# Optimization experiments

Measured on AMD Instinct MI355X. Metric: run time of the kernel, lower is better.

The kernel has to match this reference:

```python
import jax, jax.numpy as jnp
import numpy as np

B, T, C, H = 512, 1024, 64, 128


def setup_inputs() -> dict:
    key = jax.random.key(0)
    ks = jax.random.split(key, 7)
    s = 1.0 / np.sqrt(H)  # PyTorch LSTM/Linear default init U(-1/sqrt(H), 1/sqrt(H))
    u = lambda k, shape: jax.random.uniform(k, shape, jnp.float32, -s, s)
    return {
        "x": jax.random.normal(ks[0], (B, T, C), jnp.float32),
        # Per-channel stacked LSTM params; input_size=1 so W_ih is [C, 4H]
        "W_ih": u(ks[1], (C, 4 * H)),
        "W_hh": u(ks[2], (C, 4 * H, H)),
        "b_ih": u(ks[3], (C, 4 * H)),
        "b_hh": u(ks[4], (C, 4 * H)),
        # Per-channel final Linear(H, 1)
        "W_fc": u(ks[5], (C, H)),
        "b_fc": u(ks[6], (C,)),
    }


def reference(x, W_ih, W_hh, b_ih, b_hh, W_fc, b_fc):
    # x: [B, T, C]. All channels' LSTMs run as one fused vectorized scan.
    Bx, Tx, Cx = x.shape
    Hh = W_hh.shape[-1]
    b = b_ih + b_hh  # [C, 4H]
    xt = jnp.transpose(x, (1, 0, 2))  # [T, B, C]
    h0 = jnp.zeros((Bx, Cx, Hh), x.dtype)
    c0 = jnp.zeros((Bx, Cx, Hh), x.dtype)

    def step(carry, x_t):
        h, c = carry  # each [B, C, H]
        gates = (jnp.einsum('bc,cg->bcg', x_t, W_ih)
                 + jnp.einsum('bch,cgh->bcg', h, W_hh)
                 + b)  # [B, C, 4H]
        i, f, g, o = jnp.split(gates, 4, axis=-1)  # PyTorch gate order: i, f, g, o
        i = jax.nn.sigmoid(i)
        f = jax.nn.sigmoid(f)
        g = jnp.tanh(g)
        o = jax.nn.sigmoid(o)
        c = f * c + i * g
        h = o * jnp.tanh(c)
        return (h, c), None

    (h_last, _), _ = jax.lax.scan(step, (h0, c0), xt)
    # Per-channel Linear(H, 1) on the final hidden state, then squeeze -> [B, C]
    return jnp.einsum('bch,ch->bc', h_last, W_fc) + b_fc
```

## Files before the change

kernel.cpp:

```cpp
#include <hip/hip_runtime.h>


typedef _Float16 half8 __attribute__((ext_vector_type(8)));
typedef float floatx4 __attribute__((ext_vector_type(4)));

#define LOG2E 1.44269504088896340736f

__global__ __launch_bounds__(512, 2) void lstm_fused(
    const float* __restrict__ x,
    const float* __restrict__ Wih,
    const float* __restrict__ Whh,
    const float* __restrict__ bih,
    const float* __restrict__ bhh,
    const float* __restrict__ Wfc,
    const float* __restrict__ bfc,
    float* __restrict__ out)
{
    constexpr int T = 1024, C = 64, H = 128, G = 512;
    constexpr int TC = T * C;

    __shared__ _Float16 hbuf[2][8192];

    const int bid = blockIdx.x;
    const int ch  = bid & 63;
    const int b0  = (bid >> 6) << 6;

    const int tid = threadIdx.x;
    const int w   = tid >> 6;
    const int l   = tid & 63;
    const int q   = l >> 4;
    const int li  = l & 15;

    float wihr[4], bias[4];
    half8 Wf[4][4];
#pragma unroll
    for (int ct = 0; ct < 4; ++ct) {
        const float sc = (ct == 2) ? 2.0f * LOG2E : LOG2E;
        const int col = ct * H + w * 16 + li;
        wihr[ct] = Wih[ch * G + col] * sc;
        bias[ct] = (bih[ch * G + col] + bhh[ch * G + col]) * sc;
#pragma unroll
        for (int ks = 0; ks < 4; ++ks) {
            const float* wp = &Whh[((size_t)(ch * G + col)) * H + ks * 32 + q * 8];
            half8 hv;
#pragma unroll
            for (int j = 0; j < 8; ++j) hv[j] = (_Float16)(wp[j] * sc);
            Wf[ct][ks] = hv;
        }
    }

    for (int i = tid; i < 8192; i += 512) hbuf[0][i] = (_Float16)0.0f;

    float cst[4][4];
#pragma unroll
    for (int rt = 0; rt < 4; ++rt)
#pragma unroll
        for (int r = 0; r < 4; ++r) cst[rt][r] = 0.0f;

    const int ks_w = w >> 1;
    const int qq_w = ((w & 1) << 1) + (li >> 3);
    const int j_w  = li & 7;
    const int rxor = qq_w & 3;
    int wel[4];
#pragma unroll
    for (int r = 0; r < 4; ++r)
        wel[r] = ks_w * 512 + (qq_w * 16 + q * 4 + (r ^ rxor)) * 8 + j_w;
    const int rdoff = (q * 16 + (li ^ (q & 3))) * 8;

    const float* xb = x + ch;
    const int rb0 = (b0 + q * 4) * TC;

    float xv[4][4];
#pragma unroll
    for (int rt = 0; rt < 4; ++rt)
#pragma unroll
        for (int r = 0; r < 4; ++r)
            xv[rt][r] = xb[rb0 + (rt * 16 + r) * TC];

    const float* xnp   = xb + C;
    const float* xlast = xb + (T - 1) * C;

    __syncthreads();

    auto step = [&](const _Float16* __restrict__ rb, _Float16* __restrict__ wb) {
#pragma unroll
        for (int rt = 0; rt < 4; ++rt) {
            floatx4 acc[4];
#pragma unroll
            for (int ct = 0; ct < 4; ++ct)
#pragma unroll
                for (int r = 0; r < 4; ++r)
                    acc[ct][r] = fmaf(xv[rt][r], wihr[ct], bias[ct]);

#pragma unroll
            for (int ks = 0; ks < 4; ++ks) {
                const half8 a = *(const half8*)&rb[(rt * 4 + ks) * 512 + rdoff];
#pragma unroll
                for (int ct = 0; ct < 4; ++ct)
                    acc[ct] = __builtin_amdgcn_mfma_f32_16x16x32_f16(a, Wf[ct][ks], acc[ct], 0, 0, 0);
            }

#pragma unroll
            for (int r = 0; r < 4; ++r) {
                const float ig = __builtin_amdgcn_rcpf(1.0f + __builtin_amdgcn_exp2f(-acc[0][r]));
                const float fg = __builtin_amdgcn_rcpf(1.0f + __builtin_amdgcn_exp2f(-acc[1][r]));
                const float gg = 1.0f - 2.0f * __builtin_amdgcn_rcpf(1.0f + __builtin_amdgcn_exp2f(acc[2][r]));
                const float og = __builtin_amdgcn_rcpf(1.0f + __builtin_amdgcn_exp2f(-acc[3][r]));
                const float cn = fg * cst[rt][r] + ig * gg;
                cst[rt][r] = cn;
                const float tc = 1.0f - 2.0f * __builtin_amdgcn_rcpf(
                                     1.0f + __builtin_amdgcn_exp2f(cn * (2.0f * LOG2E)));
                wb[rt * 2048 + wel[r]] = (_Float16)(og * tc);
            }
        }

#pragma unroll
        for (int rt = 0; rt < 4; ++rt)
#pragma unroll
            for (int r = 0; r < 4; ++r)
                xv[rt][r] = xnp[rb0 + (rt * 16 + r) * TC];

        __syncthreads();
    };

    for (int t = 0; t < T; t += 2) {
        step(hbuf[0], hbuf[1]);
        xnp = (xnp == xlast) ? xnp : xnp + C;
        step(hbuf[1], hbuf[0]);
        xnp = (xnp == xlast) ? xnp : xnp + C;
    }

    if (tid < 64) {
        const int row = tid;
        const int rt = row >> 4, m = row & 15;
        float s = bfc[ch];
#pragma unroll
        for (int hh = 0; hh < H; ++hh) {
            const int ks = hh >> 5, qq = (hh & 31) >> 3, j = hh & 7;
            const int c = qq * 16 + (m ^ (qq & 3));
            s += (float)hbuf[0][(rt * 4 + ks) * 512 + c * 8 + j] * Wfc[ch * H + hh];
        }
        out[(size_t)(b0 + row) * C + ch] = s;
    }
}

extern "C" void kernel_launch(void* const* d_in, const int* in_sizes, int n_in,
                              void* d_out, int out_size, void* d_ws, size_t ws_size,
                              hipStream_t stream) {
    const float* x   = (const float*)d_in[0];
    const float* Wih = (const float*)d_in[1];
    const float* Whh = (const float*)d_in[2];
    const float* bih = (const float*)d_in[3];
    const float* bhh = (const float*)d_in[4];
    const float* Wfc = (const float*)d_in[5];
    const float* bfc = (const float*)d_in[6];
    float* out = (float*)d_out;

    lstm_fused<<<512, 512, 0, stream>>>(x, Wih, Whh, bih, bhh, Wfc, bfc, out);
}
```

Before: 6.371 ms.

## Stage per-step x through shared memory and share one reciprocal across gates

Only the first wave now loads the next timestep's x values, one per batch row, and writes them into a double-buffered shared array. Every thread then reads its four values as a vector from shared memory, which replaces the 16 redundant global loads per thread per step. The gate nonlinearities are rewritten to combine the four sigmoid/tanh denominators into a single reciprocal plus multiplies, with a clamp on the cell tanh argument. This reduces transcendental instructions but risks overflow in the product of denominators when gate pre-activations are large.

```diff
diff --git a/kernel.cpp b/kernel.cpp
--- a/kernel.cpp
+++ b/kernel.cpp
@@ -20,6 +20,7 @@
     constexpr int TC = T * C;
 
     __shared__ _Float16 hbuf[2][8192];
+    __shared__ float xstage[2][64];
 
     const int bid = blockIdx.x;
     const int ch  = bid & 63;
@@ -51,6 +52,9 @@
 
     for (int i = tid; i < 8192; i += 512) hbuf[0][i] = (_Float16)0.0f;
 
+    const float* xrow = x + (size_t)(b0 + (tid & 63)) * TC + ch;
+    if (tid < 64) xstage[0][tid] = xrow[0];
+
     float cst[4][4];
 #pragma unroll
     for (int rt = 0; rt < 4; ++rt)
@@ -67,30 +71,24 @@
         wel[r] = ks_w * 512 + (qq_w * 16 + q * 4 + (r ^ rxor)) * 8 + j_w;
     const int rdoff = (q * 16 + (li ^ (q & 3))) * 8;
 
-    const float* xb = x + ch;
-    const int rb0 = (b0 + q * 4) * TC;
-
-    float xv[4][4];
-#pragma unroll
-    for (int rt = 0; rt < 4; ++rt)
-#pragma unroll
-        for (int r = 0; r < 4; ++r)
-            xv[rt][r] = xb[rb0 + (rt * 16 + r) * TC];
-
-    const float* xnp   = xb + C;
-    const float* xlast = xb + (T - 1) * C;
-
     __syncthreads();
 
-    auto step = [&](const _Float16* __restrict__ rb, _Float16* __restrict__ wb) {
+    auto step = [&](const _Float16* __restrict__ rb, _Float16* __restrict__ wb,
+                    const float* __restrict__ xcur, float* __restrict__ xnxt,
+                    int tn) {
+        float xpre;
+        if (tid < 64) xpre = xrow[tn * C];
+
 #pragma unroll
         for (int rt = 0; rt < 4; ++rt) {
+            const floatx4 xq = *(const floatx4*)&xcur[rt * 16 + q * 4];
+
             floatx4 acc[4];
 #pragma unroll
             for (int ct = 0; ct < 4; ++ct)
 #pragma unroll
                 for (int r = 0; r < 4; ++r)
-                    acc[ct][r] = fmaf(xv[rt][r], wihr[ct], bias[ct]);
+                    acc[ct][r] = fmaf(xq[r], wihr[ct], bias[ct]);
 
 #pragma unroll
             for (int ks = 0; ks < 4; ++ks) {
@@ -102,32 +100,37 @@
 
 #pragma unroll
             for (int r = 0; r < 4; ++r) {
-                const float ig = __builtin_amdgcn_rcpf(1.0f + __builtin_amdgcn_exp2f(-acc[0][r]));
-                const float fg = __builtin_amdgcn_rcpf(1.0f + __builtin_amdgcn_exp2f(-acc[1][r]));
-                const float gg = 1.0f - 2.0f * __builtin_amdgcn_rcpf(1.0f + __builtin_amdgcn_exp2f(acc[2][r]));
-                const float og = __builtin_amdgcn_rcpf(1.0f + __builtin_amdgcn_exp2f(-acc[3][r]));
-                const float cn = fg * cst[rt][r] + ig * gg;
+                const float u  = __builtin_amdgcn_exp2f(-acc[0][r]);
+                const float v  = __builtin_amdgcn_exp2f(-acc[1][r]);
+                const float p  = __builtin_amdgcn_exp2f(acc[2][r]);
+                const float wq = __builtin_amdgcn_exp2f(-acc[3][r]);
+                const float Du = 1.0f + u, Dv = 1.0f + v;
+                const float Dp = 1.0f + p, Dw = 1.0f + wq;
+                const float A  = Du * Dv, Bq = Dp * Dw;
+                const float R  = __builtin_amdgcn_rcpf(A * Bq);
+                const float RA = R * Bq;
+                const float RB = R * A;
+                const float ig = Dv * RA;
+                const float fg = Du * RA;
+                const float tg = fmaf(-2.0f, Dw * RB, 1.0f);
+                const float og = Dp * RB;
+                const float cn = fmaf(fg, cst[rt][r], ig * tg);
                 cst[rt][r] = cn;
-                const float tc = 1.0f - 2.0f * __builtin_amdgcn_rcpf(
-                                     1.0f + __builtin_amdgcn_exp2f(cn * (2.0f * LOG2E)));
-                wb[rt * 2048 + wel[r]] = (_Float16)(og * tc);
+                const float tq = __builtin_amdgcn_fmed3f(
+                    cn * (2.0f * LOG2E), -29.0f, 29.0f);
+                const float hq = fmaf(-2.0f,
+                    __builtin_amdgcn_rcpf(1.0f + __builtin_amdgcn_exp2f(tq)), 1.0f);
+                wb[rt * 2048 + wel[r]] = (_Float16)(og * hq);
             }
         }
 
-#pragma unroll
-        for (int rt = 0; rt < 4; ++rt)
-#pragma unroll
-            for (int r = 0; r < 4; ++r)
-                xv[rt][r] = xnp[rb0 + (rt * 16 + r) * TC];
-
+        if (tid < 64) xnxt[tid] = xpre;
         __syncthreads();
     };
 
     for (int t = 0; t < T; t += 2) {
-        step(hbuf[0], hbuf[1]);
-        xnp = (xnp == xlast) ? xnp : xnp + C;
-        step(hbuf[1], hbuf[0]);
-        xnp = (xnp == xlast) ? xnp : xnp + C;
+        step(hbuf[0], hbuf[1], xstage[0], xstage[1], t + 1);
+        step(hbuf[1], hbuf[0], xstage[1], xstage[0], (t + 2 < T) ? t + 2 : T - 1);
     }
 
     if (tid < 64) {
```

New measurement: 6.196 ms. 1.03x faster.

## Share one reciprocal across four gate activations and vectorize gate math

Applied to the files above, without the earlier changes.

Each gate's own reciprocal is replaced by a single reciprocal of the product of the four denominators; each gate is then recovered with multiplies. This cuts transcendental rcp calls per element from five to two. The pointwise math uses floatx4 vectors so the compiler can emit packed FP32 ops, and launch bounds drop to one block per SM to free registers. The product of denominators can overflow when gate pre-activations are large. The tanh input is clamped, but the sigmoid exponentials are not, so accuracy for extreme values is at risk.

```diff
diff --git a/kernel.cpp b/kernel.cpp
--- a/kernel.cpp
+++ b/kernel.cpp
@@ -6,7 +6,7 @@
 
 #define LOG2E 1.44269504088896340736f
 
-__global__ __launch_bounds__(512, 2) void lstm_fused(
+__global__ __launch_bounds__(512, 1) void lstm_fused(
     const float* __restrict__ x,
     const float* __restrict__ Wih,
     const float* __restrict__ Whh,
@@ -51,11 +51,9 @@
 
     for (int i = tid; i < 8192; i += 512) hbuf[0][i] = (_Float16)0.0f;
 
-    float cst[4][4];
+    floatx4 cstv[4];
 #pragma unroll
-    for (int rt = 0; rt < 4; ++rt)
-#pragma unroll
-        for (int r = 0; r < 4; ++r) cst[rt][r] = 0.0f;
+    for (int rt = 0; rt < 4; ++rt) cstv[rt] = (floatx4){0.0f, 0.0f, 0.0f, 0.0f};
 
     const int ks_w = w >> 1;
     const int qq_w = ((w & 1) << 1) + (li >> 3);
@@ -70,7 +68,7 @@
     const float* xb = x + ch;
     const int rb0 = (b0 + q * 4) * TC;
 
-    float xv[4][4];
+    floatx4 xv[4];
 #pragma unroll
     for (int rt = 0; rt < 4; ++rt)
 #pragma unroll
@@ -82,15 +80,22 @@
 
     __syncthreads();
 
+    const floatx4 one   = {1.0f, 1.0f, 1.0f, 1.0f};
+    const floatx4 ntwo  = {-2.0f, -2.0f, -2.0f, -2.0f};
+    const floatx4 clo   = {-29.0f, -29.0f, -29.0f, -29.0f};
+    const floatx4 chi   = {29.0f, 29.0f, 29.0f, 29.0f};
+    const floatx4 two_l = {2.0f * LOG2E, 2.0f * LOG2E, 2.0f * LOG2E, 2.0f * LOG2E};
+
     auto step = [&](const _Float16* __restrict__ rb, _Float16* __restrict__ wb) {
 #pragma unroll
         for (int rt = 0; rt < 4; ++rt) {
             floatx4 acc[4];
 #pragma unroll
-            for (int ct = 0; ct < 4; ++ct)
-#pragma unroll
-                for (int r = 0; r < 4; ++r)
-                    acc[ct][r] = fmaf(xv[rt][r], wihr[ct], bias[ct]);
+            for (int ct = 0; ct < 4; ++ct) {
+                const floatx4 wsp = {wihr[ct], wihr[ct], wihr[ct], wihr[ct]};
+                const floatx4 bsp = {bias[ct], bias[ct], bias[ct], bias[ct]};
+                acc[ct] = __builtin_elementwise_fma(xv[rt], wsp, bsp);
+            }
 
 #pragma unroll
             for (int ks = 0; ks < 4; ++ks) {
@@ -100,18 +105,41 @@
                     acc[ct] = __builtin_amdgcn_mfma_f32_16x16x32_f16(a, Wf[ct][ks], acc[ct], 0, 0, 0);
             }
 
+            floatx4 u, v, p, wq;
 #pragma unroll
-            for (int r = 0; r < 4; ++r) {
-                const float ig = __builtin_amdgcn_rcpf(1.0f + __builtin_amdgcn_exp2f(-acc[0][r]));
-                const float fg = __builtin_amdgcn_rcpf(1.0f + __builtin_amdgcn_exp2f(-acc[1][r]));
-                const float gg = 1.0f - 2.0f * __builtin_amdgcn_rcpf(1.0f + __builtin_amdgcn_exp2f(acc[2][r]));
-                const float og = __builtin_amdgcn_rcpf(1.0f + __builtin_amdgcn_exp2f(-acc[3][r]));
-                const float cn = fg * cst[rt][r] + ig * gg;
-                cst[rt][r] = cn;
-                const float tc = 1.0f - 2.0f * __builtin_amdgcn_rcpf(
-                                     1.0f + __builtin_amdgcn_exp2f(cn * (2.0f * LOG2E)));
-                wb[rt * 2048 + wel[r]] = (_Float16)(og * tc);
+            for (int e = 0; e < 4; ++e) {
+                u[e]  = __builtin_amdgcn_exp2f(-acc[0][e]);
+                v[e]  = __builtin_amdgcn_exp2f(-acc[1][e]);
+                p[e]  = __builtin_amdgcn_exp2f(acc[2][e]);
+                wq[e] = __builtin_amdgcn_exp2f(-acc[3][e]);
             }
+            const floatx4 Du = u + one, Dv = v + one, Dp = p + one, Dw = wq + one;
+            const floatx4 A  = Du * Dv, Bq = Dp * Dw;
+            const floatx4 AB = A * Bq;
+            floatx4 R;
+#pragma unroll
+            for (int e = 0; e < 4; ++e) R[e] = __builtin_amdgcn_rcpf(AB[e]);
+            const floatx4 RA = R * Bq;
+            const floatx4 RB = R * A;
+            const floatx4 ig = Dv * RA;
+            const floatx4 fg = Du * RA;
+            const floatx4 tg = __builtin_elementwise_fma(ntwo, Dw * RB, one);
+            const floatx4 og = Dp * RB;
+            const floatx4 cn = __builtin_elementwise_fma(fg, cstv[rt], ig * tg);
+            cstv[rt] = cn;
+            floatx4 tq = cn * two_l;
+            tq = __builtin_elementwise_min(__builtin_elementwise_max(tq, clo), chi);
+            floatx4 Eq;
+#pragma unroll
+            for (int e = 0; e < 4; ++e) Eq[e] = __builtin_amdgcn_exp2f(tq[e]);
+            const floatx4 Dq = Eq + one;
+            floatx4 iq;
+#pragma unroll
+            for (int e = 0; e < 4; ++e) iq[e] = __builtin_amdgcn_rcpf(Dq[e]);
+            const floatx4 hv4 = og * __builtin_elementwise_fma(ntwo, iq, one);
+#pragma unroll
+            for (int r = 0; r < 4; ++r)
+                wb[rt * 2048 + wel[r]] = (_Float16)hv4[r];
         }
 
 #pragma unroll
```

After: 6.757 ms. 1.06x slower.
